# Optimization experiments

Measured on AMD Instinct MI355X. Metric: run time of the kernel, lower is better.

The kernel has to match this reference:

```python
import jax, jax.numpy as jnp
import numpy as np
import math

QK_DIM = 128

def setup_inputs() -> dict:
    key = jax.random.key(0)
    kx, kq, kk, kv = jax.random.split(key, 4)
    B, S, D, H = 4, 4096, 1024, 128
    X = jax.random.normal(kx, (B, S, D), dtype=jnp.float32)
    # xavier-normal-ish scale for weights
    std = math.sqrt(2.0 / (D + H))
    W_q = jax.random.normal(kq, (D, H), dtype=jnp.float32) * std
    W_k = jax.random.normal(kk, (D, H), dtype=jnp.float32) * std
    W_v = jax.random.normal(kv, (D, H), dtype=jnp.float32) * std
    return {"X": X, "W_q": W_q, "W_k": W_k, "W_v": W_v}

def reference(X, W_q, W_k, W_v):
    # X: [B, S, D]; single-head causal attention
    Q = X @ W_q                       # [B, S, H]
    K = X @ W_k                       # [B, S, H]
    V = X @ W_v                       # [B, S, H]
    S_len = X.shape[1]
    scores = jnp.einsum('bsh,bth->bst', Q, K) / math.sqrt(QK_DIM)  # [B, S, S]
    causal = jnp.tril(jnp.ones((S_len, S_len), dtype=bool))
    scores = jnp.where(causal, scores, -jnp.inf)
    attn = jax.nn.softmax(scores, axis=-1)
    return jnp.einsum('bst,bth->bsh', attn, V)
```

## Files before the change

### kernel.cpp

```cpp
#include <hip/hip_runtime.h>
#include <hip/hip_bf16.h>

#define B_ 4
#define S_ 4096
#define D_ 1024
#define H_ 128

typedef unsigned short u16;
typedef unsigned int u32;
typedef short s16x8 __attribute__((ext_vector_type(8)));
typedef float f32x4 __attribute__((ext_vector_type(4)));

__device__ __forceinline__ u16 f2bf(float f) {
    u32 x = __float_as_uint(f);
    u32 r = x + 0x7fffu + ((x >> 16) & 1u);
    return (u16)(r >> 16);
}

__device__ __forceinline__ void gl_lds16(const u16* g, u16* l) {
    __builtin_amdgcn_global_load_lds(
        (const __attribute__((address_space(1))) u32*)g,
        (__attribute__((address_space(3))) u32*)l, 16, 0, 0);
}

__global__ void detect_dtype_kernel(const u32* __restrict__ w, int* __restrict__ flag) {
    __shared__ int smax[256];
    const int tid = threadIdx.x;
    int m = 0;
    for (int i = tid; i < 1024; i += 256) {
        u32 x = w[i];
        m = max(m, max((int)((x >> 7) & 0xFF), (int)((x >> 23) & 0xFF)));
    }
    smax[tid] = m;
    __syncthreads();
    if (tid == 0) {
        int mm = 0;
        for (int i = 0; i < 256; ++i) mm = max(mm, smax[i]);
        *flag = (mm >= 200) ? 1 : 0;
    }
}

__global__ __launch_bounds__(256) void prep_w_kernel(
    const void* __restrict__ Wq, const void* __restrict__ Wk, const void* __restrict__ Wv,
    u16* __restrict__ Wt, const int* __restrict__ dflag)
{
    const int kt = blockIdx.x, mat = blockIdx.y;
    const void* W = (mat == 0) ? Wq : (mat == 1) ? Wk : Wv;
    const int isf = *dflag;
    const int t = threadIdx.x;
    const int kk = t >> 3;
    const int n0 = (t & 7) * 16;
    u16 vals[16];
    if (isf) {
        const float* wp = (const float*)W + (size_t)(kt * 32 + kk) * H_ + n0;
#pragma unroll
        for (int i = 0; i < 16; ++i) vals[i] = f2bf(wp[i]);
    } else {
        const u16* wp = (const u16*)W + (size_t)(kt * 32 + kk) * H_ + n0;
#pragma unroll
        for (int i = 0; i < 16; ++i) vals[i] = wp[i];
    }
    const size_t base = (size_t)(mat * 32 + kt) * 128;
#pragma unroll
    for (int i = 0; i < 16; ++i)
        Wt[(base + n0 + i) * 32 + kk] = vals[i];
}

__global__ __launch_bounds__(256) void qkv_kernel(
    const void* __restrict__ Xv, const u16* __restrict__ Wt,
    u16* __restrict__ Qo, u16* __restrict__ Ko, u16* __restrict__ Vto,
    const int* __restrict__ dflag)
{
    __shared__ u16 Ws[2][384 * 32];
    __shared__ union { u16 qk[32 * 136]; u16 vt[128 * 40]; } OsU;

    const int isf = *dflag;
    const int tid = threadIdx.x;
    const int w = tid >> 6, lane = tid & 63;
    const int r = lane & 15, q = lane >> 4;
    const size_t m0 = (size_t)blockIdx.x * 32;

    f32x4 acc[2][6];
#pragma unroll
    for (int s2 = 0; s2 < 2; ++s2)
#pragma unroll
        for (int i = 0; i < 6; ++i) acc[s2][i] = (f32x4){0.f, 0.f, 0.f, 0.f};

    const float* xf0 = (const float*)Xv + (m0 + r) * D_;
    const float* xf1 = (const float*)Xv + (m0 + 16 + r) * D_;
    const u16*   xb0 = (const u16*)Xv + (m0 + r) * D_;
    const u16*   xb1 = (const u16*)Xv + (m0 + 16 + r) * D_;

    float4 af[2][2];
    uint4  ab[2];

#pragma unroll
    for (int i = 0; i < 6; ++i) {
        int c = tid + i * 256;
        gl_lds16(Wt + (size_t)((c >> 9) * 32) * 4096 + (c & 511) * 8, &Ws[0][c * 8]);
    }
    if (isf) {
        af[0][0] = *(const float4*)(xf0 + q * 8);
        af[0][1] = *(const float4*)(xf0 + q * 8 + 4);
        af[1][0] = *(const float4*)(xf1 + q * 8);
        af[1][1] = *(const float4*)(xf1 + q * 8 + 4);
    } else {
        ab[0] = *(const uint4*)(xb0 + q * 8);
        ab[1] = *(const uint4*)(xb1 + q * 8);
    }

    for (int kt = 0; kt < 32; ++kt) {
        const int buf = kt & 1;
        __syncthreads();

        if (kt + 1 < 32) {
#pragma unroll
            for (int i = 0; i < 6; ++i) {
                int c = tid + i * 256;
                gl_lds16(Wt + (size_t)((c >> 9) * 32 + kt + 1) * 4096 + (c & 511) * 8,
                         &Ws[buf ^ 1][c * 8]);
            }
        }

        s16x8 a[2];
        if (isf) {
#pragma unroll
            for (int s2 = 0; s2 < 2; ++s2) {
                union { u16 u[8]; s16x8 v; } pk;
                pk.u[0] = f2bf(af[s2][0].x); pk.u[1] = f2bf(af[s2][0].y);
                pk.u[2] = f2bf(af[s2][0].z); pk.u[3] = f2bf(af[s2][0].w);
                pk.u[4] = f2bf(af[s2][1].x); pk.u[5] = f2bf(af[s2][1].y);
                pk.u[6] = f2bf(af[s2][1].z); pk.u[7] = f2bf(af[s2][1].w);
                a[s2] = pk.v;
            }
        } else {
            a[0] = *(const s16x8*)&ab[0];
            a[1] = *(const s16x8*)&ab[1];
        }

        if (kt + 1 < 32) {
            const int k0 = (kt + 1) * 32;
            if (isf) {
                af[0][0] = *(const float4*)(xf0 + k0 + q * 8);
                af[0][1] = *(const float4*)(xf0 + k0 + q * 8 + 4);
                af[1][0] = *(const float4*)(xf1 + k0 + q * 8);
                af[1][1] = *(const float4*)(xf1 + k0 + q * 8 + 4);
            } else {
                ab[0] = *(const uint4*)(xb0 + k0 + q * 8);
                ab[1] = *(const uint4*)(xb1 + k0 + q * 8);
            }
        }

#pragma unroll
        for (int i = 0; i < 6; ++i) {
            int c = w * 6 + i;
            s16x8 b = *(const s16x8*)&Ws[buf][(c >> 3) * 4096 + ((c & 7) * 16 + r) * 32 + q * 8];
            acc[0][i] = __builtin_amdgcn_mfma_f32_16x16x32_bf16(a[0], b, acc[0][i], 0, 0, 0);
            acc[1][i] = __builtin_amdgcn_mfma_f32_16x16x32_bf16(a[1], b, acc[1][i], 0, 0, 0);
        }
    }

    u16* outs[2] = {Qo, Ko};
    for (int m = 0; m < 2; ++m) {
        const float sc = (m == 0) ? 0.08838834764831845f : 1.0f;
        __syncthreads();
#pragma unroll
        for (int i = 0; i < 6; ++i) {
            int c = w * 6 + i;
            if ((c >> 3) == m) {
                int nt = c & 7;
#pragma unroll
                for (int s2 = 0; s2 < 2; ++s2)
#pragma unroll
                    for (int reg = 0; reg < 4; ++reg)
                        OsU.qk[(s2 * 16 + q * 4 + reg) * 136 + nt * 16 + r] = f2bf(acc[s2][i][reg] * sc);
            }
        }
        __syncthreads();
        u16* Out = outs[m];
#pragma unroll
        for (int it = 0; it < 2; ++it) {
            int c = tid + it * 256;
            int row = c >> 4, col = (c & 15) * 8;
            *(uint4*)(Out + (m0 + row) * H_ + col) = *(const uint4*)&OsU.qk[row * 136 + col];
        }
    }

    __syncthreads();
#pragma unroll
    for (int i = 0; i < 6; ++i) {
        int c = w * 6 + i;
        if ((c >> 3) == 2) {
            int nt = c & 7;
#pragma unroll
            for (int s2 = 0; s2 < 2; ++s2)
#pragma unroll
                for (int reg = 0; reg < 4; ++reg)
                    OsU.vt[(nt * 16 + r) * 40 + s2 * 16 + q * 4 + reg] = f2bf(acc[s2][i][reg]);
        }
    }
    __syncthreads();
    {
        const int bb = blockIdx.x >> 7;
        const int s0 = (blockIdx.x & 127) * 32;
#pragma unroll
        for (int it = 0; it < 2; ++it) {
            int c = tid + it * 256;
            int h = c >> 2, sh = (c & 3) * 8;
            *(uint4*)(Vto + ((size_t)bb * H_ + h) * S_ + s0 + sh) =
                *(const uint4*)&OsU.vt[h * 40 + sh];
        }
    }
}

__global__ __launch_bounds__(256) void attn_kernel(
    const u16* __restrict__ Q, const u16* __restrict__ K, const u16* __restrict__ Vt,
    void* __restrict__ out, const int* __restrict__ dflag)
{
    __shared__ union {
        u16 ps[2][32 * 136];
        float of[32 * 132];
    } U;
    __shared__ float lsumS[4][32];

    const int isf = *dflag;
    const int tid = threadIdx.x;
    const int w = tid >> 6, lane = tid & 63;
    const int r = lane & 15, q = lane >> 4;
    const int bid = blockIdx.x;
    const int b = bid & 3;
    const int qt = (bid < 256) ? (bid >> 2) : (127 - ((bid - 256) >> 2));

    const u16* Qg  = Q  + ((size_t)b * S_ + (size_t)qt * 32) * H_;
    const u16* Kg  = K  + (size_t)b * S_ * H_;
    const u16* Vtg = Vt + (size_t)b * H_ * S_;

    s16x8 qf[2][4];
#pragma unroll
    for (int M = 0; M < 2; ++M)
#pragma unroll
        for (int ks = 0; ks < 4; ++ks)
            qf[M][ks] = *(const s16x8*)(Qg + (size_t)(M * 16 + r) * H_ + ks * 32 + q * 8);

    float lp[2][4];
#pragma unroll
    for (int M = 0; M < 2; ++M)
#pragma unroll
        for (int reg = 0; reg < 4; ++reg) lp[M][reg] = 0.f;

    f32x4 accO[2][2];
#pragma unroll
    for (int M = 0; M < 2; ++M)
#pragma unroll
        for (int ht = 0; ht < 2; ++ht) accO[M][ht] = (f32x4){0.f, 0.f, 0.f, 0.f};

    const int nKT = (qt >> 2) + 1;

    s16x8 kf[2][4];
#pragma unroll
    for (int t2 = 0; t2 < 2; ++t2)
#pragma unroll
        for (int ks = 0; ks < 4; ++ks)
            kf[t2][ks] = *(const s16x8*)(Kg + (size_t)(w * 32 + t2 * 16 + r) * H_ + ks * 32 + q * 8);

    for (int j = 0; j < nKT; ++j) {
        f32x4 accS[2][2];
#pragma unroll
        for (int M = 0; M < 2; ++M)
#pragma unroll
            for (int t2 = 0; t2 < 2; ++t2) accS[M][t2] = (f32x4){0.f, 0.f, 0.f, 0.f};
#pragma unroll
        for (int ks = 0; ks < 4; ++ks)
#pragma unroll
            for (int t2 = 0; t2 < 2; ++t2)
#pragma unroll
                for (int M = 0; M < 2; ++M)
                    accS[M][t2] = __builtin_amdgcn_mfma_f32_16x16x32_bf16(qf[M][ks], kf[t2][ks], accS[M][t2], 0, 0, 0);

        s16x8 vf[2][4];
#pragma unroll
        for (int ht = 0; ht < 2; ++ht)
#pragma unroll
            for (int ks = 0; ks < 4; ++ks)
                vf[ht][ks] = *(const s16x8*)(Vtg + (size_t)(w * 32 + ht * 16 + r) * S_ + (size_t)j * 128 + ks * 32 + q * 8);

        const bool last = (j == nKT - 1);
        const int key0 = j * 128 + w * 32 + r;
        u16* psb = &U.ps[j & 1][0];
#pragma unroll
        for (int M = 0; M < 2; ++M)
#pragma unroll
            for (int t2 = 0; t2 < 2; ++t2)
#pragma unroll
                for (int reg = 0; reg < 4; ++reg) {
                    int key = key0 + t2 * 16;
                    int grow = qt * 32 + M * 16 + q * 4 + reg;
                    float s = fminf(accS[M][t2][reg], 80.f);
                    float p = __expf(s);
                    if (last && key > grow) p = 0.f;
                    lp[M][reg] += p;
                    psb[(M * 16 + q * 4 + reg) * 136 + w * 32 + t2 * 16 + r] = f2bf(p);
                }
        __syncthreads();

        if (j + 1 < nKT) {
#pragma unroll
            for (int t2 = 0; t2 < 2; ++t2)
#pragma unroll
                for (int ks = 0; ks < 4; ++ks)
                    kf[t2][ks] = *(const s16x8*)(Kg + ((size_t)(j + 1) * 128 + w * 32 + t2 * 16 + r) * H_ + ks * 32 + q * 8);
        }

#pragma unroll
        for (int ks = 0; ks < 4; ++ks) {
            s16x8 pa0 = *(const s16x8*)&psb[(size_t)(r) * 136 + ks * 32 + q * 8];
            s16x8 pa1 = *(const s16x8*)&psb[(size_t)(16 + r) * 136 + ks * 32 + q * 8];
#pragma unroll
            for (int ht = 0; ht < 2; ++ht) {
                accO[0][ht] = __builtin_amdgcn_mfma_f32_16x16x32_bf16(pa0, vf[ht][ks], accO[0][ht], 0, 0, 0);
                accO[1][ht] = __builtin_amdgcn_mfma_f32_16x16x32_bf16(pa1, vf[ht][ks], accO[1][ht], 0, 0, 0);
            }
        }
    }

#pragma unroll
    for (int M = 0; M < 2; ++M)
#pragma unroll
        for (int reg = 0; reg < 4; ++reg) {
            float v = lp[M][reg];
            v += __shfl_xor(v, 1);
            v += __shfl_xor(v, 2);
            v += __shfl_xor(v, 4);
            v += __shfl_xor(v, 8);
            lp[M][reg] = v;
        }
    if (r == 0) {
#pragma unroll
        for (int M = 0; M < 2; ++M)
#pragma unroll
            for (int reg = 0; reg < 4; ++reg)
                lsumS[w][M * 16 + q * 4 + reg] = lp[M][reg];
    }
    __syncthreads();

    float linv[2][4];
#pragma unroll
    for (int M = 0; M < 2; ++M)
#pragma unroll
        for (int reg = 0; reg < 4; ++reg) {
            int row = M * 16 + q * 4 + reg;
            linv[M][reg] = 1.0f / (lsumS[0][row] + lsumS[1][row] + lsumS[2][row] + lsumS[3][row]);
        }

#pragma unroll
    for (int M = 0; M < 2; ++M)
#pragma unroll
        for (int ht = 0; ht < 2; ++ht)
#pragma unroll
            for (int reg = 0; reg < 4; ++reg)
                U.of[(M * 16 + q * 4 + reg) * 132 + w * 32 + ht * 16 + r] = accO[M][ht][reg] * linv[M][reg];
    __syncthreads();
    {
        const size_t obase = (size_t)b * S_ + (size_t)qt * 32;
        int row = tid >> 3, col = (tid & 7) * 16;
        const float* src = &U.of[row * 132 + col];
        if (isf) {
            float* dst = (float*)out + (obase + row) * H_ + col;
#pragma unroll
            for (int i = 0; i < 4; ++i)
                *(float4*)(dst + i * 4) = *(const float4*)(src + i * 4);
        } else {
            u16* dst = (u16*)out + (obase + row) * H_ + col;
#pragma unroll
            for (int hh = 0; hh < 2; ++hh) {
                union { u16 u[8]; uint4 v; } pk;
#pragma unroll
                for (int i = 0; i < 8; ++i) pk.u[i] = f2bf(src[hh * 8 + i]);
                *(uint4*)(dst + hh * 8) = pk.v;
            }
        }
    }
}

extern "C" void kernel_launch(void* const* d_in, const int* in_sizes, int n_in,
                              void* d_out, int out_size, void* d_ws, size_t ws_size,
                              hipStream_t stream) {
    (void)in_sizes; (void)n_in; (void)out_size; (void)ws_size;
    const void* X  = d_in[0];
    const void* Wq = d_in[1];
    const void* Wk = d_in[2];
    const void* Wv = d_in[3];

    int* dflag = (int*)d_ws;
    u16* Qw = (u16*)((char*)d_ws + 256);
    const size_t n = (size_t)B_ * S_ * H_;
    u16* Kw = Qw + n;
    u16* Vtw = Kw + n;
    u16* Wt = Vtw + n;

    detect_dtype_kernel<<<1, 256, 0, stream>>>((const u32*)Wq, dflag);
    prep_w_kernel<<<dim3(32, 3), 256, 0, stream>>>(Wq, Wk, Wv, Wt, dflag);
    qkv_kernel<<<512, 256, 0, stream>>>(X, Wt, Qw, Kw, Vtw, dflag);
    attn_kernel<<<512, 256, 0, stream>>>(Qw, Kw, Vtw, d_out, dflag);
}
```

Baseline: 213.0 us.

## Split key blocks across waves with 32x32 MFMA and register-resident P

Restructures the attention kernel so that each of the four waves handles a strided subset of 32-key blocks for all 32 query rows. It computes S^T with 32x32x16 MFMAs and turns the probabilities into the PV operand in registers using cvt_pk_bf16 and permlane32_swap, so P no longer goes through LDS. The per-block __syncthreads is gone, but the four waves' partial outputs and row sums must now be reduced through a larger 64KB LDS buffer at the end. The larger LDS footprint and register use may lower occupancy.

```diff
diff --git a/kernel.cpp b/kernel.cpp
--- a/kernel.cpp
+++ b/kernel.cpp
@@ -10,11 +10,21 @@
 typedef unsigned int u32;
 typedef short s16x8 __attribute__((ext_vector_type(8)));
 typedef float f32x4 __attribute__((ext_vector_type(4)));
+typedef float f32x16 __attribute__((ext_vector_type(16)));
 
 __device__ __forceinline__ u16 f2bf(float f) {
     u32 x = __float_as_uint(f);
     u32 r = x + 0x7fffu + ((x >> 16) & 1u);
     return (u16)(r >> 16);
+}
+
+__device__ __forceinline__ u32 cvtpk_bf16(float a, float b) {
+    u32 r;
+    asm("v_cvt_pk_bf16_f32 %0, %1, %2" : "=v"(r) : "v"(a), "v"(b));
+    return r;
+}
+__device__ __forceinline__ void pl32swap(u32& x, u32& y) {
+    asm("v_permlane32_swap_b32 %0, %1" : "+v"(x), "+v"(y));
 }
 
 __device__ __forceinline__ void gl_lds16(const u16* g, u16* l) {
@@ -217,16 +227,13 @@
     const u16* __restrict__ Q, const u16* __restrict__ K, const u16* __restrict__ Vt,
     void* __restrict__ out, const int* __restrict__ dflag)
 {
-    __shared__ union {
-        u16 ps[2][32 * 136];
-        float of[32 * 132];
-    } U;
-    __shared__ float lsumS[4][32];
+    __shared__ float opS[4][32][128];
+    __shared__ float lpS[4][32];
 
     const int isf = *dflag;
     const int tid = threadIdx.x;
     const int w = tid >> 6, lane = tid & 63;
-    const int r = lane & 15, q = lane >> 4;
+    const int l31 = lane & 31, hi = lane >> 5;
     const int bid = blockIdx.x;
     const int b = bid & 3;
     const int qt = (bid < 256) ? (bid >> 2) : (127 - ((bid - 256) >> 2));
@@ -235,147 +242,118 @@
     const u16* Kg  = K  + (size_t)b * S_ * H_;
     const u16* Vtg = Vt + (size_t)b * H_ * S_;
 
-    s16x8 qf[2][4];
-#pragma unroll
-    for (int M = 0; M < 2; ++M)
-#pragma unroll
-        for (int ks = 0; ks < 4; ++ks)
-            qf[M][ks] = *(const s16x8*)(Qg + (size_t)(M * 16 + r) * H_ + ks * 32 + q * 8);
-
-    float lp[2][4];
-#pragma unroll
-    for (int M = 0; M < 2; ++M)
-#pragma unroll
-        for (int reg = 0; reg < 4; ++reg) lp[M][reg] = 0.f;
-
-    f32x4 accO[2][2];
-#pragma unroll
-    for (int M = 0; M < 2; ++M)
-#pragma unroll
-        for (int ht = 0; ht < 2; ++ht) accO[M][ht] = (f32x4){0.f, 0.f, 0.f, 0.f};
-
-    const int nKT = (qt >> 2) + 1;
-
-    s16x8 kf[2][4];
-#pragma unroll
-    for (int t2 = 0; t2 < 2; ++t2)
-#pragma unroll
-        for (int ks = 0; ks < 4; ++ks)
-            kf[t2][ks] = *(const s16x8*)(Kg + (size_t)(w * 32 + t2 * 16 + r) * H_ + ks * 32 + q * 8);
-
-    for (int j = 0; j < nKT; ++j) {
-        f32x4 accS[2][2];
-#pragma unroll
-        for (int M = 0; M < 2; ++M)
-#pragma unroll
-            for (int t2 = 0; t2 < 2; ++t2) accS[M][t2] = (f32x4){0.f, 0.f, 0.f, 0.f};
-#pragma unroll
-        for (int ks = 0; ks < 4; ++ks)
-#pragma unroll
-            for (int t2 = 0; t2 < 2; ++t2)
-#pragma unroll
-                for (int M = 0; M < 2; ++M)
-                    accS[M][t2] = __builtin_amdgcn_mfma_f32_16x16x32_bf16(qf[M][ks], kf[t2][ks], accS[M][t2], 0, 0, 0);
-
-        s16x8 vf[2][4];
-#pragma unroll
-        for (int ht = 0; ht < 2; ++ht)
-#pragma unroll
-            for (int ks = 0; ks < 4; ++ks)
-                vf[ht][ks] = *(const s16x8*)(Vtg + (size_t)(w * 32 + ht * 16 + r) * S_ + (size_t)j * 128 + ks * 32 + q * 8);
-
-        const bool last = (j == nKT - 1);
-        const int key0 = j * 128 + w * 32 + r;
-        u16* psb = &U.ps[j & 1][0];
-#pragma unroll
-        for (int M = 0; M < 2; ++M)
-#pragma unroll
-            for (int t2 = 0; t2 < 2; ++t2)
-#pragma unroll
-                for (int reg = 0; reg < 4; ++reg) {
-                    int key = key0 + t2 * 16;
-                    int grow = qt * 32 + M * 16 + q * 4 + reg;
-                    float s = fminf(accS[M][t2][reg], 80.f);
-                    float p = __expf(s);
-                    if (last && key > grow) p = 0.f;
-                    lp[M][reg] += p;
-                    psb[(M * 16 + q * 4 + reg) * 136 + w * 32 + t2 * 16 + r] = f2bf(p);
-                }
-        __syncthreads();
-
-        if (j + 1 < nKT) {
-#pragma unroll
-            for (int t2 = 0; t2 < 2; ++t2)
-#pragma unroll
-                for (int ks = 0; ks < 4; ++ks)
-                    kf[t2][ks] = *(const s16x8*)(Kg + ((size_t)(j + 1) * 128 + w * 32 + t2 * 16 + r) * H_ + ks * 32 + q * 8);
-        }
-
-#pragma unroll
-        for (int ks = 0; ks < 4; ++ks) {
-            s16x8 pa0 = *(const s16x8*)&psb[(size_t)(r) * 136 + ks * 32 + q * 8];
-            s16x8 pa1 = *(const s16x8*)&psb[(size_t)(16 + r) * 136 + ks * 32 + q * 8];
-#pragma unroll
-            for (int ht = 0; ht < 2; ++ht) {
-                accO[0][ht] = __builtin_amdgcn_mfma_f32_16x16x32_bf16(pa0, vf[ht][ks], accO[0][ht], 0, 0, 0);
-                accO[1][ht] = __builtin_amdgcn_mfma_f32_16x16x32_bf16(pa1, vf[ht][ks], accO[1][ht], 0, 0, 0);
-            }
-        }
-    }
-
-#pragma unroll
-    for (int M = 0; M < 2; ++M)
-#pragma unroll
-        for (int reg = 0; reg < 4; ++reg) {
-            float v = lp[M][reg];
-            v += __shfl_xor(v, 1);
-            v += __shfl_xor(v, 2);
-            v += __shfl_xor(v, 4);
-            v += __shfl_xor(v, 8);
-            lp[M][reg] = v;
-        }
-    if (r == 0) {
-#pragma unroll
-        for (int M = 0; M < 2; ++M)
-#pragma unroll
-            for (int reg = 0; reg < 4; ++reg)
-                lsumS[w][M * 16 + q * 4 + reg] = lp[M][reg];
-    }
+    s16x8 qf[8];
+#pragma unroll
+    for (int sl = 0; sl < 8; ++sl)
+        qf[sl] = *(const s16x8*)(Qg + (size_t)l31 * H_ + sl * 16 + hi * 8);
+
+    f32x16 accO[4];
+#pragma unroll
+    for (int hg = 0; hg < 4; ++hg)
+#pragma unroll
+        for (int i = 0; i < 16; ++i) accO[hg][i] = 0.f;
+    float lp = 0.f;
+
+    s16x8 kf[8];
+    if (w <= qt) {
+#pragma unroll
+        for (int sl = 0; sl < 8; ++sl)
+            kf[sl] = *(const s16x8*)(Kg + ((size_t)w * 32 + l31) * H_ + sl * 16 + hi * 8);
+    }
+
+    for (int c = w; c <= qt; c += 4) {
+        const int kb = c * 32;
+
+        s16x8 vf[4][2];
+#pragma unroll
+        for (int hg = 0; hg < 4; ++hg)
+#pragma unroll
+            for (int ks = 0; ks < 2; ++ks)
+                vf[hg][ks] = *(const s16x8*)(Vtg + (size_t)(hg * 32 + l31) * S_ + kb + ks * 16 + hi * 8);
+
+        f32x16 sacc;
+#pragma unroll
+        for (int i = 0; i < 16; ++i) sacc[i] = 0.f;
+#pragma unroll
+        for (int sl = 0; sl < 8; ++sl)
+            sacc = __builtin_amdgcn_mfma_f32_32x32x16_bf16(kf[sl], qf[sl], sacc, 0, 0, 0);
+
+        if (c + 4 <= qt) {
+#pragma unroll
+            for (int sl = 0; sl < 8; ++sl)
+                kf[sl] = *(const s16x8*)(Kg + ((size_t)(kb + 128) + l31) * H_ + sl * 16 + hi * 8);
+        }
+
+        const bool diag = (c == qt);
+        float p[16];
+#pragma unroll
+        for (int r = 0; r < 16; ++r) {
+            float s = fminf(sacc[r], 80.f);
+            float pv = __expf(s);
+            if (diag && ((r & 3) + 8 * (r >> 2) + 4 * hi) > l31) pv = 0.f;
+            lp += pv;
+            p[r] = pv;
+        }
+
+        u32 w01 = cvtpk_bf16(p[0], p[1]),  w23 = cvtpk_bf16(p[2], p[3]);
+        u32 w45 = cvtpk_bf16(p[4], p[5]),  w67 = cvtpk_bf16(p[6], p[7]);
+        pl32swap(w01, w45);
+        pl32swap(w23, w67);
+        u32 x01 = cvtpk_bf16(p[8], p[9]),  x23 = cvtpk_bf16(p[10], p[11]);
+        u32 x45 = cvtpk_bf16(p[12], p[13]), x67 = cvtpk_bf16(p[14], p[15]);
+        pl32swap(x01, x45);
+        pl32swap(x23, x67);
+        union { u32 u[4]; s16x8 v; } pa0, pa1;
+        pa0.u[0] = w01; pa0.u[1] = w23; pa0.u[2] = w45; pa0.u[3] = w67;
+        pa1.u[0] = x01; pa1.u[1] = x23; pa1.u[2] = x45; pa1.u[3] = x67;
+
+#pragma unroll
+        for (int hg = 0; hg < 4; ++hg) {
+            accO[hg] = __builtin_amdgcn_mfma_f32_32x32x16_bf16(pa0.v, vf[hg][0], accO[hg], 0, 0, 0);
+            accO[hg] = __builtin_amdgcn_mfma_f32_32x32x16_bf16(pa1.v, vf[hg][1], accO[hg], 0, 0, 0);
+        }
+    }
+
+    lp += __shfl_xor(lp, 32);
+
+#pragma unroll
+    for (int hg = 0; hg < 4; ++hg)
+#pragma unroll
+        for (int r = 0; r < 16; ++r)
+            opS[w][(r & 3) + 8 * (r >> 2) + 4 * hi][hg * 32 + l31] = accO[hg][r];
+    if (lane < 32) lpS[w][l31] = lp;
     __syncthreads();
 
-    float linv[2][4];
-#pragma unroll
-    for (int M = 0; M < 2; ++M)
-#pragma unroll
-        for (int reg = 0; reg < 4; ++reg) {
-            int row = M * 16 + q * 4 + reg;
-            linv[M][reg] = 1.0f / (lsumS[0][row] + lsumS[1][row] + lsumS[2][row] + lsumS[3][row]);
-        }
-
-#pragma unroll
-    for (int M = 0; M < 2; ++M)
-#pragma unroll
-        for (int ht = 0; ht < 2; ++ht)
-#pragma unroll
-            for (int reg = 0; reg < 4; ++reg)
-                U.of[(M * 16 + q * 4 + reg) * 132 + w * 32 + ht * 16 + r] = accO[M][ht][reg] * linv[M][reg];
-    __syncthreads();
     {
-        const size_t obase = (size_t)b * S_ + (size_t)qt * 32;
-        int row = tid >> 3, col = (tid & 7) * 16;
-        const float* src = &U.of[row * 132 + col];
+        const int q = tid >> 3;
+        const int hs = (tid & 7) * 16;
+        const float l = lpS[0][q] + lpS[1][q] + lpS[2][q] + lpS[3][q];
+        const float inv = 1.0f / l;
+        float vals[16];
+#pragma unroll
+        for (int i = 0; i < 16; i += 4) {
+            float4 a0 = *(const float4*)&opS[0][q][hs + i];
+            float4 a1 = *(const float4*)&opS[1][q][hs + i];
+            float4 a2 = *(const float4*)&opS[2][q][hs + i];
+            float4 a3 = *(const float4*)&opS[3][q][hs + i];
+            vals[i + 0] = (a0.x + a1.x + a2.x + a3.x) * inv;
+            vals[i + 1] = (a0.y + a1.y + a2.y + a3.y) * inv;
+            vals[i + 2] = (a0.z + a1.z + a2.z + a3.z) * inv;
+            vals[i + 3] = (a0.w + a1.w + a2.w + a3.w) * inv;
+        }
+        const size_t orow = (size_t)b * S_ + (size_t)qt * 32 + q;
         if (isf) {
-            float* dst = (float*)out + (obase + row) * H_ + col;
+            float* dst = (float*)out + orow * H_ + hs;
 #pragma unroll
             for (int i = 0; i < 4; ++i)
-                *(float4*)(dst + i * 4) = *(const float4*)(src + i * 4);
+                *(float4*)(dst + i * 4) = *(const float4*)(&vals[i * 4]);
         } else {
-            u16* dst = (u16*)out + (obase + row) * H_ + col;
+            u16* dst = (u16*)out + orow * H_ + hs;
 #pragma unroll
             for (int hh = 0; hh < 2; ++hh) {
                 union { u16 u[8]; uint4 v; } pk;
 #pragma unroll
-                for (int i = 0; i < 8; ++i) pk.u[i] = f2bf(src[hh * 8 + i]);
+                for (int i = 0; i < 8; ++i) pk.u[i] = f2bf(vals[hh * 8 + i]);
                 *(uint4*)(dst + hh * 8) = pk.v;
             }
         }
```

Measured after the change: 207.1 us. 1.03x faster.
